# Kernel tuning notes

Hardware: AMD Instinct MI355X
Metric: run time of the kernel (lower is better)

## Reference

```python
import jax, jax.numpy as jnp
import numpy as np

B = 8
NUM_CLASSES = 80
STRIDES = (8, 16, 32, 64, 128)
HS = (96, 48, 24, 12, 6)
WS = (160, 80, 40, 20, 10)
IMG_H, IMG_W = 768, 1280
OCTAVE_SCALE = 4.0
LOC_THR = 0.01
SCORE_THR = 0.05
IOU_THR = 0.5
NMS_PRE = 1000
MAX_PER_IMG = 100
MAX_RATIO_ANCHOR = abs(float(np.log(1e-6)))        # anchor_coder wh_ratio_clip=1e-6
MAX_RATIO_BBOX = abs(float(np.log(16.0 / 1000.0)))  # bbox_coder default wh_ratio_clip
CLS_OFFSET = 4096.0  # > max image coord, separates classes for class-aware NMS


def setup_inputs():
    inp = {}
    k = 0
    for i, (h, w) in enumerate(zip(HS, WS)):
        for name, c in (("cls_score", NUM_CLASSES), ("bbox_pred", 4), ("shape_pred", 2), ("loc_pred", 1)):
            k += 1
            inp[f"{name}_{i}"] = jax.random.normal(jax.random.fold_in(jax.random.key(0), k), (B, c, h, w), dtype=jnp.float32)
    return inp


def _squares(h, w, stride):
    # mmdet square anchor generator: base size stride*octave_base_scale, ratio 1, center offset 0
    xs = jnp.arange(w, dtype=jnp.float32) * stride
    ys = jnp.arange(h, dtype=jnp.float32) * stride
    yy, xx = jnp.meshgrid(ys, xs, indexing="ij")
    half = 0.5 * OCTAVE_SCALE * stride
    return jnp.stack([xx - half, yy - half, xx + half, yy + half], -1).reshape(-1, 4)


def _delta2bbox(rois, deltas, max_ratio, max_shape=None):
    dx, dy = deltas[..., 0], deltas[..., 1]
    dw = jnp.clip(deltas[..., 2], -max_ratio, max_ratio)
    dh = jnp.clip(deltas[..., 3], -max_ratio, max_ratio)
    px = (rois[..., 0] + rois[..., 2]) * 0.5
    py = (rois[..., 1] + rois[..., 3]) * 0.5
    pw = rois[..., 2] - rois[..., 0]
    ph = rois[..., 3] - rois[..., 1]
    gx = px + pw * dx
    gy = py + ph * dy
    gw = pw * jnp.exp(dw)
    gh = ph * jnp.exp(dh)
    x1, y1 = gx - 0.5 * gw, gy - 0.5 * gh
    x2, y2 = gx + 0.5 * gw, gy + 0.5 * gh
    if max_shape is not None:
        x1 = jnp.clip(x1, 0.0, float(max_shape[1]))
        x2 = jnp.clip(x2, 0.0, float(max_shape[1]))
        y1 = jnp.clip(y1, 0.0, float(max_shape[0]))
        y2 = jnp.clip(y2, 0.0, float(max_shape[0]))
    return jnp.stack([x1, y1, x2, y2], -1)


def _level(cls, bbox, shp, loc, stride, h, w):
    b = cls.shape[0]
    # NOTE: double sigmoid is faithful to the original wrapper (it sigmoids twice)
    scores = jax.nn.sigmoid(jax.nn.sigmoid(jnp.transpose(cls, (0, 2, 3, 1)).reshape(b, -1, NUM_CLASSES)))
    mask = (jax.nn.sigmoid(loc) >= LOC_THR).astype(scores.dtype)
    mask = jnp.transpose(mask, (0, 2, 3, 1)).reshape(b, -1)  # num_anchors == 1
    scores = scores * mask[:, :, None]
    deltas = jnp.transpose(shp, (0, 2, 3, 1)).reshape(b, -1, 2)
    bdel = jnp.concatenate([jnp.zeros_like(deltas), deltas], axis=-1)  # [0,0,dw,dh]
    anchors = _delta2bbox(_squares(h, w, stride)[None], bdel, MAX_RATIO_ANCHOR)  # guided anchors
    bbox = jnp.transpose(bbox, (0, 2, 3, 1)).reshape(b, -1, 4)
    n = scores.shape[1]
    if n < NMS_PRE:  # pad_with_value
        pad = NMS_PRE - n
        scores = jnp.pad(scores, ((0, 0), (0, pad), (0, 0)))
        bbox = jnp.pad(bbox, ((0, 0), (0, pad), (0, 0)))
        anchors = jnp.pad(anchors, ((0, 0), (0, pad), (0, 0)))
    _, idx = jax.lax.top_k(scores.max(-1), NMS_PRE)
    scores = jnp.take_along_axis(scores, idx[:, :, None], axis=1)
    bbox = jnp.take_along_axis(bbox, idx[:, :, None], axis=1)
    anchors = jnp.take_along_axis(anchors, idx[:, :, None], axis=1)
    proposals = _delta2bbox(anchors, bbox, MAX_RATIO_BBOX, (IMG_H, IMG_W))
    return scores, proposals


def _iou_one_vs_all(box, boxes):
    lt = jnp.maximum(box[:2], boxes[:, :2])
    rb = jnp.minimum(box[2:], boxes[:, 2:])
    wh = jnp.clip(rb - lt, 0.0, None)
    inter = wh[:, 0] * wh[:, 1]
    a1 = (box[2] - box[0]) * (box[3] - box[1])
    a2 = (boxes[:, 2] - boxes[:, 0]) * (boxes[:, 3] - boxes[:, 1])
    return inter / (a1 + a2 - inter + 1e-6)


def _nms_single(scores, boxes):
    # class-aware greedy NMS (BatchedNMS semantics): scores [N,C], boxes [N,4]
    n, c = scores.shape
    s = jnp.where(scores > SCORE_THR, scores, 0.0).reshape(-1)  # [N*C]
    offs = (jnp.arange(c, dtype=boxes.dtype) * CLS_OFFSET)[None, :, None]
    cboxes = (boxes[:, None, :] + offs).reshape(-1, 4)  # class-offset boxes

    def step(sv, _):
        i = jnp.argmax(sv)
        sc = sv[i]
        keep = sc > 0.0
        iou = _iou_one_vs_all(cboxes[i], cboxes)
        sv = jnp.where(iou > IOU_THR, 0.0, sv)  # suppresses i itself too
        cls = jnp.where(keep, (i % c).astype(jnp.int32), -1)
        return sv, (boxes[i // c], sc, cls, keep)

    _, (ob, osc, ocls, okeep) = jax.lax.scan(step, s, None, length=MAX_PER_IMG)
    kf = okeep.astype(boxes.dtype)
    return okeep.sum().astype(jnp.int32), ob * kf[:, None], osc * kf, ocls


def _forward(tensors):
    mlvl_scores, mlvl_props = [], []
    for i in range(5):
        s, p = _level(tensors[4 * i], tensors[4 * i + 1], tensors[4 * i + 2], tensors[4 * i + 3],
                      STRIDES[i], HS[i], WS[i])
        mlvl_scores.append(s)
        mlvl_props.append(p)
    scores = jnp.concatenate(mlvl_scores, axis=1)   # [B, 5000, 80]
    props = jnp.concatenate(mlvl_props, axis=1)     # [B, 5000, 4]
    k = min(max(1000, NMS_PRE), scores.shape[1])
    _, idx = jax.lax.top_k(scores.max(-1), k)
    scores = jnp.take_along_axis(scores, idx[:, :, None], axis=1)
    props = jnp.take_along_axis(props, idx[:, :, None], axis=1)
    return jax.vmap(_nms_single)(scores, props)


def reference(cls_score_0, bbox_pred_0, shape_pred_0, loc_pred_0,
              cls_score_1, bbox_pred_1, shape_pred_1, loc_pred_1,
              cls_score_2, bbox_pred_2, shape_pred_2, loc_pred_2,
              cls_score_3, bbox_pred_3, shape_pred_3, loc_pred_3,
              cls_score_4, bbox_pred_4, shape_pred_4, loc_pred_4):
    tensors = [cls_score_0, bbox_pred_0, shape_pred_0, loc_pred_0,
               cls_score_1, bbox_pred_1, shape_pred_1, loc_pred_1,
               cls_score_2, bbox_pred_2, shape_pred_2, loc_pred_2,
               cls_score_3, bbox_pred_3, shape_pred_3, loc_pred_3,
               cls_score_4, bbox_pred_4, shape_pred_4, loc_pred_4]
    num_detected, proposals, out_scores, cls_id = _forward(tensors)
    return num_detected, proposals, out_scores, cls_id
```

## Files before the change

### kernel.cpp

```cpp
#include <hip/hip_runtime.h>
#include <stdint.h>

#define NCLS 80
#define BATCH 8
#define NA 20460
#define TOPK 1000
#define MAXPER 100
#define CAP 8
#define POOL 256
#define IMG_WF 1280.0f
#define IMG_HF 768.0f
#define CLS_OFF 4096.0f
#define MAX_RATIO_ANCHOR 13.815510557964274f
#define MAX_RATIO_BBOX   4.1351665567423557f

#define K2_HALF_UP (0.5 + 0x1p-25)

__constant__ int   c_lvoff[6]  = {0, 15360, 19200, 20160, 20400, 20460};
__constant__ int   c_lvoff4[6] = {0, 3840, 4800, 5040, 5100, 5115};
__constant__ int   c_lw[5]    = {160, 80, 40, 20, 10};
__constant__ int   c_lh[5]    = {96, 48, 24, 12, 6};
__constant__ float c_ls[5]    = {8.f, 16.f, 32.f, 64.f, 128.f};

struct InPtrs {
  const float* cls[5];
  const float* bbox[5];
  const float* shp[5];
  const float* loc[5];
};

__device__ __forceinline__ float sigf(float x) { return 1.0f / (1.0f + expf(-x)); }

__device__ __forceinline__ int wave_red_sum_i32(int v) {
  int t;
  t = __builtin_amdgcn_update_dpp(0, v, 0x111, 0xf, 0xf, false); v += t;
  t = __builtin_amdgcn_update_dpp(0, v, 0x112, 0xf, 0xf, false); v += t;
  t = __builtin_amdgcn_update_dpp(0, v, 0x114, 0xf, 0xf, false); v += t;
  t = __builtin_amdgcn_update_dpp(0, v, 0x118, 0xf, 0xf, false); v += t;
  t = __builtin_amdgcn_update_dpp(0, v, 0x142, 0xf, 0xf, false); v += t;
  t = __builtin_amdgcn_update_dpp(0, v, 0x143, 0xf, 0xf, false); v += t;
  return __builtin_amdgcn_readlane(v, 63);
}
__device__ __forceinline__ void wave_red_top2(unsigned m1, unsigned m2,
                                              unsigned& r1, unsigned& r2) {
#define T2STEP(ctrl) { \
    unsigned o1 = (unsigned)__builtin_amdgcn_update_dpp(0, (int)m1, ctrl, 0xf, 0xf, false); \
    unsigned o2 = (unsigned)__builtin_amdgcn_update_dpp(0, (int)m2, ctrl, 0xf, 0xf, false); \
    unsigned tm = min(m1, o1); \
    m1 = max(m1, o1); \
    m2 = max(tm, max(m2, o2)); }
  T2STEP(0x111) T2STEP(0x112) T2STEP(0x114) T2STEP(0x118) T2STEP(0x142) T2STEP(0x143)
#undef T2STEP
  r1 = (unsigned)__builtin_amdgcn_readlane((int)m1, 63);
  r2 = (unsigned)__builtin_amdgcn_readlane((int)m2, 63);
}

__global__ __launch_bounds__(256) void k_score(InPtrs P, unsigned* wkeys, unsigned* hist) {
  int gid = blockIdx.x * 256 + threadIdx.x;
  if (gid >= BATCH * (NA / 4)) return;
  int b = gid / (NA / 4);
  int q = gid - b * (NA / 4);
  int l = 0;
  while (q >= c_lvoff4[l + 1]) ++l;
  int hw = c_lh[l] * c_lw[l];
  int sp = (q - c_lvoff4[l]) * 4;
  const float4* cls = (const float4*)(P.cls[l] + (size_t)(b * NCLS) * hw + sp);
  int s4 = hw >> 2;
  float4 m = cls[0];
  for (int c = 1; c < NCLS; ++c) {
    float4 v = cls[(size_t)c * s4];
    m.x = fmaxf(m.x, v.x); m.y = fmaxf(m.y, v.y);
    m.z = fmaxf(m.z, v.z); m.w = fmaxf(m.w, v.w);
  }
  float4 lo = *(const float4*)(P.loc[l] + (size_t)b * hw + sp);
  float4 r;
  r.x = (sigf(lo.x) >= 0.01f) ? sigf(sigf(m.x)) : 0.0f;
  r.y = (sigf(lo.y) >= 0.01f) ? sigf(sigf(m.y)) : 0.0f;
  r.z = (sigf(lo.z) >= 0.01f) ? sigf(sigf(m.z)) : 0.0f;
  r.w = (sigf(lo.w) >= 0.01f) ? sigf(sigf(m.w)) : 0.0f;
  uint4 wq;
  wq.x = __float_as_uint(r.x) & 0x3FFFFFu;
  wq.y = __float_as_uint(r.y) & 0x3FFFFFu;
  wq.z = __float_as_uint(r.z) & 0x3FFFFFu;
  wq.w = __float_as_uint(r.w) & 0x3FFFFFu;
  ((uint4*)wkeys)[(size_t)b * (NA / 4) + q] = wq;
  unsigned* hb = hist + b * 2048;
  atomicAdd(&hb[wq.x >> 11], 1u);
  atomicAdd(&hb[wq.y >> 11], 1u);
  atomicAdd(&hb[wq.z >> 11], 1u);
  atomicAdd(&hb[wq.w >> 11], 1u);
}

__global__ __launch_bounds__(1024) void k_select(const unsigned* wkeys, const unsigned* hist,
                                                 int* sel) {
  int b = blockIdx.x;
  int tid = threadIdx.x;
  int wv = tid >> 6;
  int lane = tid & 63;
  __shared__ unsigned s_h[2048];
  __shared__ int s_wtot[16];
  __shared__ int s_res[2];
  __shared__ unsigned long long s_A[1024];
  __shared__ unsigned long long s_B[1024];

  const int NAq = NA / 4;
  unsigned w[20];
  #pragma unroll
  for (int k = 0; k < 5; ++k) {
    int q = tid * 5 + k;
    uint4 u = (q < NAq) ? ((const uint4*)wkeys)[(size_t)b * NAq + q]
                        : make_uint4(0u, 0u, 0u, 0u);
    w[k * 4 + 0] = u.x;
    w[k * 4 + 1] = u.y;
    w[k * 4 + 2] = u.z;
    w[k * 4 + 3] = u.w;
  }
  int lim = NA - tid * 20;
  lim = (lim < 0) ? 0 : ((lim > 20) ? 20 : lim);

  s_h[tid] = hist[b * 2048 + tid];
  s_h[tid + 1024] = hist[b * 2048 + 1024 + tid];
  __syncthreads();

  auto scanFind = [&](int target) {
    int b0 = 2047 - 2 * tid;
    int h0 = (int)s_h[b0];
    int h1 = (int)s_h[b0 - 1];
    int pair = h0 + h1;
    int incl = pair;
    #pragma unroll
    for (int o = 1; o < 64; o <<= 1) {
      int uu = __shfl_up(incl, o, 64);
      if (lane >= o) incl += uu;
    }
    if (lane == 63) s_wtot[wv] = incl;
    __syncthreads();
    int woff = 0;
    #pragma unroll
    for (int ww = 0; ww < 16; ++ww) woff += (ww < wv) ? s_wtot[ww] : 0;
    int excl = woff + incl - pair;
    if (excl < target && excl + h0 >= target) { s_res[0] = b0; s_res[1] = excl; }
    int e1 = excl + h0;
    if (e1 < target && e1 + h1 >= target) { s_res[0] = b0 - 1; s_res[1] = e1; }
    __syncthreads();
  };

  scanFind(TOPK);
  int B1 = s_res[0];
  int NGT1 = s_res[1];

  s_h[tid] = 0u; s_h[tid + 1024] = 0u;
  __syncthreads();
  #pragma unroll
  for (int k = 0; k < 20; ++k)
    if ((int)(w[k] >> 11) == B1) atomicAdd(&s_h[w[k] & 0x7FFu], 1u);
  __syncthreads();
  scanFind(TOPK - NGT1);
  unsigned V = ((unsigned)B1 << 11) | (unsigned)s_res[0];

  if (tid < 1024 - TOPK) s_A[TOPK + tid] = 0ull;

  int cgt = 0;
  #pragma unroll
  for (int k = 0; k < 20; ++k) cgt += (w[k] > V) ? 1 : 0;
  {
    int incl = cgt;
    #pragma unroll
    for (int o = 1; o < 64; o <<= 1) {
      int uu = __shfl_up(incl, o, 64);
      if (lane >= o) incl += uu;
    }
    if (lane == 63) s_wtot[wv] = incl;
    __syncthreads();
    int woff = 0, tot = 0;
    #pragma unroll
    for (int ww = 0; ww < 16; ++ww) { tot += s_wtot[ww]; woff += (ww < wv) ? s_wtot[ww] : 0; }
    int pos = woff + incl - cgt;
    #pragma unroll
    for (int k = 0; k < 20; ++k) {
      if (w[k] > V) {
        int i = tid * 20 + k;
        s_A[pos++] = ((unsigned long long)w[k] << 32) |
                     (unsigned long long)(0xFFFFFFFFu - (unsigned)i);
      }
    }
    int ngt = tot;
    int need = TOPK - ngt;
    __syncthreads();

    int ceq = 0;
    #pragma unroll
    for (int k = 0; k < 20; ++k) if (k < lim && w[k] == V) ++ceq;
    int incl2 = ceq;
    #pragma unroll
    for (int o = 1; o < 64; o <<= 1) {
      int uu = __shfl_up(incl2, o, 64);
      if (lane >= o) incl2 += uu;
    }
    if (lane == 63) s_wtot[wv] = incl2;
    __syncthreads();
    int woff2 = 0;
    #pragma unroll
    for (int ww = 0; ww < 16; ++ww) woff2 += (ww < wv) ? s_wtot[ww] : 0;
    int r = woff2 + incl2 - ceq;
    #pragma unroll
    for (int k = 0; k < 20; ++k) {
      if (k < lim && w[k] == V) {
        if (r < need) {
          int i = tid * 20 + k;
          s_A[ngt + r] = ((unsigned long long)V << 32) |
                         (unsigned long long)(0xFFFFFFFFu - (unsigned)i);
        }
        ++r;
      }
    }
  }
  __syncthreads();

  unsigned long long key = s_A[tid];
  int tog = 0;
  for (unsigned k = 2; k <= 1024; k <<= 1) {
    for (unsigned j = k >> 1; j > 0; j >>= 1) {
      unsigned long long other;
      if (j >= 64) {
        unsigned long long* cur = tog ? s_A : s_B;
        cur[tid] = key;
        __syncthreads();
        other = cur[tid ^ (int)j];
        tog ^= 1;
      } else {
        other = __shfl_xor(key, (int)j, 64);
      }
      bool takeMax = (((tid & (int)k) == 0) == ((tid & (int)j) == 0));
      unsigned long long mx = (key > other) ? key : other;
      unsigned long long mn = (key > other) ? other : key;
      key = takeMax ? mx : mn;
    }
  }
  if (tid < TOPK) {
    sel[b * TOPK + tid] = (int)(0xFFFFFFFFu - (unsigned)(key & 0xFFFFFFFFull));
  }
}

__global__ __launch_bounds__(256) void k_gather(InPtrs P, const int* sel, float* boxes, float* sv) {
  int wvi = threadIdx.x >> 6;
  int lane = threadIdx.x & 63;
  int wid = blockIdx.x * 4 + wvi;
  int b = wid / TOPK;
  int r = wid - b * TOPK;
  __shared__ float s_sc[4][NCLS];

  int a = sel[b * TOPK + r];
  int l = 0;
  while (a >= c_lvoff[l + 1]) ++l;
  int within = a - c_lvoff[l];
  int W = c_lw[l], H = c_lh[l];
  int y = within / W, x = within - y * W;
  int hw = H * W;
  int sp = within;
  float stride = c_ls[l];
  float px = (float)x * stride;
  float py = (float)y * stride;
  float pw = 4.0f * stride;

  const float* shp = P.shp[l];
  float dws = shp[(b * 2 + 0) * hw + sp];
  float dhs = shp[(b * 2 + 1) * hw + sp];
  dws = fminf(fmaxf(dws, -MAX_RATIO_ANCHOR), MAX_RATIO_ANCHOR);
  dhs = fminf(fmaxf(dhs, -MAX_RATIO_ANCHOR), MAX_RATIO_ANCHOR);
  float gw = pw * expf(dws);
  float gh = pw * expf(dhs);
  float ax1 = px - 0.5f * gw, ax2 = px + 0.5f * gw;
  float ay1 = py - 0.5f * gh, ay2 = py + 0.5f * gh;

  const float* bb = P.bbox[l];
  float dx = bb[(b * 4 + 0) * hw + sp];
  float dy = bb[(b * 4 + 1) * hw + sp];
  float dw = bb[(b * 4 + 2) * hw + sp];
  float dh = bb[(b * 4 + 3) * hw + sp];
  dw = fminf(fmaxf(dw, -MAX_RATIO_BBOX), MAX_RATIO_BBOX);
  dh = fminf(fmaxf(dh, -MAX_RATIO_BBOX), MAX_RATIO_BBOX);
  float px2 = (ax1 + ax2) * 0.5f, py2 = (ay1 + ay2) * 0.5f;
  float pw2 = ax2 - ax1, ph2 = ay2 - ay1;
  float gx = px2 + pw2 * dx, gy = py2 + ph2 * dy;
  float gw2 = pw2 * expf(dw), gh2 = ph2 * expf(dh);
  float x1 = fminf(fmaxf(gx - 0.5f * gw2, 0.0f), IMG_WF);
  float x2 = fminf(fmaxf(gx + 0.5f * gw2, 0.0f), IMG_WF);
  float y1 = fminf(fmaxf(gy - 0.5f * gh2, 0.0f), IMG_HF);
  float y2 = fminf(fmaxf(gy + 0.5f * gh2, 0.0f), IMG_HF);
  if (lane == 0) {
    float4 st; st.x = x1; st.y = y1; st.z = x2; st.w = y2;
    ((float4*)boxes)[b * TOPK + r] = st;
  }

  const float* cls = P.cls[l];
  float sl = sigf(P.loc[l][b * hw + sp]);
  bool mask = (sl >= 0.01f);
  int base = (b * NCLS) * hw + sp;
  for (int c = lane; c < NCLS; c += 64) {
    float vv = 0.0f;
    if (mask) {
      float s2 = sigf(sigf(cls[base + c * hw]));
      vv = (s2 > 0.05f) ? s2 : 0.0f;
    }
    s_sc[wvi][c] = vv;
  }
  __syncthreads();
  int t = threadIdx.x;
  if (t < NCLS) {
    int r0 = blockIdx.x * 4 - b * TOPK;
    float4 o; o.x = s_sc[0][t]; o.y = s_sc[1][t]; o.z = s_sc[2][t]; o.w = s_sc[3][t];
    *(float4*)(sv + ((size_t)(b * NCLS + t) * TOPK + r0)) = o;
  }
}

__global__ __launch_bounds__(256) void k_nms(const float* boxes, const float* sv,
                                             float* keptScore, int* keptRow, int* kc,
                                             const int* flags, const int* gbits, int cap) {
  int bc = blockIdx.x;
  if (flags && flags[bc] == 0) return;
  int b = bc / NCLS;
  int c = bc - b * NCLS;
  int tid = threadIdx.x;
  int wv = tid >> 6, lane = tid & 63;

  unsigned Glow = 0u;
  if (gbits) Glow = ((unsigned)gbits[b]) & 0x3FFFFFu;

  __shared__ float4 s_box[TOPK];
  __shared__ float  s_ard[TOPK];
  __shared__ unsigned long long s_p2[2][4];

  float x1[4], y1[4], x2[4], y2[4], ar[4];
  unsigned key[4];
  float off = (float)c * CLS_OFF;
  const float* svc = sv + (size_t)(b * NCLS + c) * TOPK;
  #pragma unroll
  for (int j = 0; j < 4; ++j) {
    int row = j * 256 + tid;
    if (row < TOPK) {
      float4 bo = ((const float4*)boxes)[b * TOPK + row];
      float a = bo.x + off, d = bo.y + off, e = bo.z + off, f = bo.w + off;
      x1[j] = a; y1[j] = d; x2[j] = e; y2[j] = f;
      ar[j] = (e - a) * (f - d);
      unsigned bits = __float_as_uint(svc[row]);
      key[j] = ((bits & 0x3FFFFFu) << 10) | (1023u - (unsigned)row);
      float sden = ar[j] + 1e-6f;
      bool deg = !((double)ar[j] > (double)sden * K2_HALF_UP);
      float4 sb; sb.x = a; sb.y = d; sb.z = e; sb.w = f;
      s_box[row] = sb;
      s_ard[row] = __uint_as_float(__float_as_uint(ar[j]) | (deg ? 0x80000000u : 0u));
    } else {
      x1[j] = y1[j] = x2[j] = y2[j] = ar[j] = 0.0f;
      key[j] = 0u;
    }
  }
  __syncthreads();

  int kept = 0;
  bool sticky = false;
  float* ks = keptScore + (size_t)(b * NCLS + c) * MAXPER;
  int*   kr = keptRow   + (size_t)(b * NCLS + c) * MAXPER;

  for (int round = 0; round < cap; ++round) {
    int par = round & 1;
    unsigned hi1 = max(key[0], key[1]), lo1 = min(key[0], key[1]);
    unsigned hi2 = max(key[2], key[3]), lo2 = min(key[2], key[3]);
    unsigned m1 = max(hi1, hi2);
    unsigned m2 = max(min(hi1, hi2), max(lo1, lo2));
    unsigned w1, w2;
    wave_red_top2(m1, m2, w1, w2);
    if (lane == 0) s_p2[par][wv] = ((unsigned long long)w1 << 32) | w2;
    __syncthreads();
    unsigned k0 = 0u, k1 = 0u;
    #pragma unroll
    for (int w = 0; w < 4; ++w) {
      unsigned long long pp = s_p2[par][w];
      unsigned p1 = (unsigned)(pp >> 32), p2 = (unsigned)pp;
      unsigned tm = min(k0, p1);
      k0 = max(k0, p1);
      k1 = max(tm, max(k1, p2));
    }
    if (k0 < 1024u) break;
    if ((k0 >> 10) < Glow) break;
    int brow1 = 1023 - (int)(k0 & 1023u);
    float bs1 = __uint_as_float(0x3F000000u | (k0 >> 10));
    float4 bb1 = s_box[brow1];
    unsigned au1 = __float_as_uint(s_ard[brow1]);
    bool deg1 = (au1 >> 31) != 0u;
    float ba1 = __uint_as_float(au1 & 0x7FFFFFFFu);
    if (tid == 0) { ks[kept] = bs1; kr[kept] = brow1; }
    kept++;
    if (deg1) { sticky = true; break; }
    if (kept >= cap) break;
    bool live2 = (k1 >= 1024u) && ((k1 >> 10) >= Glow);
    if (!live2) break;
    bool do2 = false, deg2 = false;
    float4 bb2; float ba2 = 0.0f;
    {
      int brow2 = 1023 - (int)(k1 & 1023u);
      float bs2 = __uint_as_float(0x3F000000u | (k1 >> 10));
      bb2 = s_box[brow2];
      unsigned au2 = __float_as_uint(s_ard[brow2]);
      deg2 = (au2 >> 31) != 0u;
      ba2 = __uint_as_float(au2 & 0x7FFFFFFFu);
      float ltx = fmaxf(bb1.x, bb2.x), rbx = fminf(bb1.z, bb2.z);
      float lty = fmaxf(bb1.y, bb2.y), rby = fminf(bb1.w, bb2.w);
      float w_ = fmaxf(rbx - ltx, 0.0f), h_ = fmaxf(rby - lty, 0.0f);
      float inter = w_ * h_;
      float denom = ((ba1 + ba2) - inter) + 1e-6f;
      if (!((double)inter > (double)denom * K2_HALF_UP)) {
        do2 = true;
        if (tid == 0) { ks[kept] = bs2; kr[kept] = brow2; }
        kept++;
      }
    }
    if (do2 && deg2) { sticky = true; break; }
    #pragma unroll
    for (int j = 0; j < 4; ++j) {
      {
        float ltx = fmaxf(bb1.x, x1[j]), rbx = fminf(bb1.z, x2[j]);
        float lty = fmaxf(bb1.y, y1[j]), rby = fminf(bb1.w, y2[j]);
        float w_ = fmaxf(rbx - ltx, 0.0f), h_ = fmaxf(rby - lty, 0.0f);
        float inter = w_ * h_;
        float denom = ((ba1 + ar[j]) - inter) + 1e-6f;
        if ((double)inter > (double)denom * K2_HALF_UP) key[j] = 0u;
      }
      if (do2) {
        float ltx = fmaxf(bb2.x, x1[j]), rbx = fminf(bb2.z, x2[j]);
        float lty = fmaxf(bb2.y, y1[j]), rby = fminf(bb2.w, y2[j]);
        float w_ = fmaxf(rbx - ltx, 0.0f), h_ = fmaxf(rby - lty, 0.0f);
        float inter = w_ * h_;
        float denom = ((ba2 + ar[j]) - inter) + 1e-6f;
        if ((double)inter > (double)denom * K2_HALF_UP) key[j] = 0u;
      }
    }
    if (kept >= cap) break;
  }
  if (tid == 0) kc[b * NCLS + c] = sticky ? -kept : kept;
}

__global__ __launch_bounds__(256) void k_cut(const float* keptScore, const int* kc,
                                             int* flags, int* gbits) {
  int b = blockIdx.x;
  int tid = threadIdx.x;
  int wv = tid >> 6, lane = tid & 63;
  __shared__ int s_abs[NCLS];
  __shared__ int s_neg[NCLS];
  __shared__ unsigned s_h[2048];
  __shared__ int s_wtot[4];
  __shared__ int s_res[2];
  __shared__ int s_tot[4];

  if (tid < NCLS) {
    int v = kc[b * NCLS + tid];
    s_abs[tid] = (v < 0) ? -v : v;
    s_neg[tid] = (v < 0) ? 1 : 0;
  }
  #pragma unroll
  for (int j = 0; j < 8; ++j) s_h[tid * 8 + j] = 0u;
  __syncthreads();

  unsigned vv[3] = {0u, 0u, 0u};
  #pragma unroll
  for (int t = 0; t < 3; ++t) {
    int e = tid + t * 256;
    if (e < NCLS * CAP) {
      int c = e / CAP, k = e - c * CAP;
      if (k < s_abs[c])
        vv[t] = __float_as_uint(keptScore[(size_t)b * NCLS * MAXPER + c * MAXPER + k])
                & 0x3FFFFFu;
    }
  }
  int live = ((vv[0] != 0u) ? 1 : 0) + ((vv[1] != 0u) ? 1 : 0) + ((vv[2] != 0u) ? 1 : 0);
  live = wave_red_sum_i32(live);
  if (lane == 0) s_tot[wv] = live;
  #pragma unroll
  for (int t = 0; t < 3; ++t) if (vv[t]) atomicAdd(&s_h[vv[t] >> 11], 1u);
  __syncthreads();
  int T = s_tot[0] + s_tot[1] + s_tot[2] + s_tot[3];

  auto scanFind = [&](int target) {
    int base = 2047 - 8 * tid;
    int h[8]; int loc = 0;
    #pragma unroll
    for (int j = 0; j < 8; ++j) { h[j] = (int)s_h[base - j]; loc += h[j]; }
    int incl = loc;
    #pragma unroll
    for (int o = 1; o < 64; o <<= 1) {
      int uu = __shfl_up(incl, o, 64);
      if (lane >= o) incl += uu;
    }
    if (lane == 63) s_wtot[wv] = incl;
    __syncthreads();
    int woff = 0;
    #pragma unroll
    for (int ww = 0; ww < 4; ++ww) woff += (ww < wv) ? s_wtot[ww] : 0;
    int e = woff + incl - loc;
    #pragma unroll
    for (int j = 0; j < 8; ++j) {
      if (e < target && e + h[j] >= target) { s_res[0] = base - j; s_res[1] = e; }
      e += h[j];
    }
    __syncthreads();
  };

  unsigned G = 0u;
  if (T >= MAXPER) {
    scanFind(MAXPER);
    int B1 = s_res[0], NGT1 = s_res[1];
    #pragma unroll
    for (int j = 0; j < 8; ++j) s_h[tid * 8 + j] = 0u;
    __syncthreads();
    #pragma unroll
    for (int t = 0; t < 3; ++t)
      if (vv[t] && (int)(vv[t] >> 11) == B1) atomicAdd(&s_h[vv[t] & 0x7FFu], 1u);
    __syncthreads();
    scanFind(MAXPER - NGT1);
    G = 0x3F000000u | ((unsigned)B1 << 11) | (unsigned)s_res[0];
  }
  if (tid == 0) gbits[b] = (int)G;
  if (tid < NCLS) {
    int f = 0;
    if (s_abs[tid] == CAP && !s_neg[tid]) {
      unsigned slast = __float_as_uint(
          keptScore[(size_t)b * NCLS * MAXPER + tid * MAXPER + (CAP - 1)]);
      if (slast >= G) f = 1;
    }
    flags[b * NCLS + tid] = f;
  }
}

__global__ __launch_bounds__(256) void k_merge(const float* boxes, const float* keptScore,
                                               const int* keptRow, const int* kc, float* out) {
  int b = blockIdx.x;
  int tid = threadIdx.x;
  int wv = tid >> 6, lane = tid & 63;
  __shared__ int s_kc[NCLS];
  __shared__ unsigned s_h[2048];
  __shared__ int s_wtot[4];
  __shared__ int s_res[2];
  __shared__ int s_tot[4];
  __shared__ int s_pos;
  __shared__ int s_sticky;
  __shared__ int s_navail;
  __shared__ unsigned long long s_pool[POOL];
  __shared__ unsigned long long s_sorted[POOL];

  for (int c = tid; c < NCLS; c += 256) s_kc[c] = kc[b * NCLS + c];
  if (tid == 0) { s_pos = 0; s_sticky = 0x7FFFFFFF; s_navail = 0; }
  for (int i = tid; i < POOL; i += 256) { s_pool[i] = 0ull; s_sorted[i] = 0ull; }
  #pragma unroll
  for (int j = 0; j < 8; ++j) s_h[tid * 8 + j] = 0u;
  __syncthreads();

  unsigned sc[32];
  #pragma unroll
  for (int s = 0; s < 32; ++s) {
    int i = tid + s * 256;
    unsigned vvv = 0u;
    if (i < NCLS * MAXPER) {
      int c = i / MAXPER, k = i - c * MAXPER;
      int kcv = s_kc[c];
      int ka = (kcv < 0) ? -kcv : kcv;
      if (k < ka)
        vvv = __float_as_uint(keptScore[(size_t)b * NCLS * MAXPER + i]) & 0x3FFFFFu;
    }
    sc[s] = vvv;
  }
  int live = 0;
  #pragma unroll
  for (int s = 0; s < 32; ++s) live += (sc[s] != 0u) ? 1 : 0;
  live = wave_red_sum_i32(live);
  if (lane == 0) s_tot[wv] = live;
  #pragma unroll
  for (int s = 0; s < 32; ++s) if (sc[s]) atomicAdd(&s_h[sc[s] >> 11], 1u);
  __syncthreads();
  int T = s_tot[0] + s_tot[1] + s_tot[2] + s_tot[3];

  auto scanFind = [&](int target) {
    int base = 2047 - 8 * tid;
    int h[8]; int loc = 0;
    #pragma unroll
    for (int j = 0; j < 8; ++j) { h[j] = (int)s_h[base - j]; loc += h[j]; }
    int incl = loc;
    #pragma unroll
    for (int o = 1; o < 64; o <<= 1) {
      int uu = __shfl_up(incl, o, 64);
      if (lane >= o) incl += uu;
    }
    if (lane == 63) s_wtot[wv] = incl;
    __syncthreads();
    int woff = 0;
    #pragma unroll
    for (int ww = 0; ww < 4; ++ww) woff += (ww < wv) ? s_wtot[ww] : 0;
    int e = woff + incl - loc;
    #pragma unroll
    for (int j = 0; j < 8; ++j) {
      if (e < target && e + h[j] >= target) { s_res[0] = base - j; s_res[1] = e; }
      e += h[j];
    }
    __syncthreads();
  };

  unsigned V = 1u;
  if (T > MAXPER) {
    scanFind(MAXPER);
    int B1 = s_res[0], NGT1 = s_res[1];
    #pragma unroll
    for (int j = 0; j < 8; ++j) s_h[tid * 8 + j] = 0u;
    __syncthreads();
    #pragma unroll
    for (int s = 0; s < 32; ++s)
      if (sc[s] && (int)(sc[s] >> 11) == B1) atomicAdd(&s_h[sc[s] & 0x7FFu], 1u);
    __syncthreads();
    scanFind(MAXPER - NGT1);
    V = ((unsigned)B1 << 11) | (unsigned)s_res[0];
  }

  #pragma unroll
  for (int s = 0; s < 32; ++s) {
    if (sc[s] >= V && sc[s] != 0u) {
      int i = tid + s * 256;
      int c = i / MAXPER, k = i - c * MAXPER;
      int kcv = s_kc[c];
      int ka = (kcv < 0) ? -kcv : kcv;
      unsigned st = (kcv < 0 && k == ka - 1) ? 1u : 0u;
      unsigned row = (unsigned)keptRow[(size_t)b * NCLS * MAXPER + i];
      unsigned flat = row * 80u + (unsigned)c;
      int p = atomicAdd(&s_pos, 1);
      if (p < POOL)
        s_pool[p] = ((unsigned long long)(0x3F000000u | sc[s]) << 32) |
                    (unsigned long long)(0x7FFFFFFFu - ((flat << 1) | st));
    }
  }
  __syncthreads();

  if (tid < POOL) {
    unsigned long long mykey = s_pool[tid];
    if (mykey != 0ull) {
      int rank = 0;
      #pragma unroll 8
      for (int s = 0; s < POOL; ++s) rank += (s_pool[s] > mykey) ? 1 : 0;
      s_sorted[rank] = mykey;
    }
  }
  __syncthreads();

  if (tid < MAXPER) {
    unsigned long long key = s_sorted[tid];
    if (key != 0ull) {
      atomicAdd(&s_navail, 1);
      if ((((unsigned)key) & 1u) == 0u) atomicMin(&s_sticky, tid);
    }
  }
  __syncthreads();
  int navail = s_navail;
  int p = s_sticky;
  int n = (p < navail) ? MAXPER : navail;

  if (tid == 0) out[b] = (float)n;
  const int OB = BATCH;
  const int OP = OB + BATCH * MAXPER * 4;
  const int OS = OP + BATCH * MAXPER;
  if (tid < MAXPER) {
    int k = tid;
    float bx0 = 0.f, bx1 = 0.f, bx2 = 0.f, bx3 = 0.f, scf = 0.f, cf = -1.0f;
    if (k < n) {
      int idx = (k > p) ? p : k;
      unsigned long long key = s_sorted[idx];
      unsigned flat = (0x7FFFFFFFu - (unsigned)key) >> 1;
      unsigned cls = flat % 80u;
      unsigned row = flat / 80u;
      float4 bo = ((const float4*)boxes)[b * TOPK + row];
      bx0 = bo.x; bx1 = bo.y; bx2 = bo.z; bx3 = bo.w;
      scf = __uint_as_float((unsigned)(key >> 32));
      cf = (float)cls;
    }
    float* po = out + OB + (size_t)(b * MAXPER + k) * 4;
    po[0] = bx0; po[1] = bx1; po[2] = bx2; po[3] = bx3;
    out[OP + b * MAXPER + k] = scf;
    out[OS + b * MAXPER + k] = cf;
  }
}

extern "C" void kernel_launch(void* const* d_in, const int* in_sizes, int n_in,
                              void* d_out, int out_size, void* d_ws, size_t ws_size,
                              hipStream_t stream) {
  InPtrs P;
  for (int l = 0; l < 5; ++l) {
    P.cls[l]  = (const float*)d_in[4 * l + 0];
    P.bbox[l] = (const float*)d_in[4 * l + 1];
    P.shp[l]  = (const float*)d_in[4 * l + 2];
    P.loc[l]  = (const float*)d_in[4 * l + 3];
  }
  unsigned* wkeys  = (unsigned*)d_ws;
  unsigned* hist   = wkeys + BATCH * NA;
  int*   sel       = (int*)(hist + BATCH * 2048);
  float* boxes     = (float*)(sel + BATCH * TOPK);
  float* sv        = boxes + BATCH * TOPK * 4;
  float* keptScore = sv + BATCH * NCLS * TOPK;
  int*   keptRow   = (int*)(keptScore + BATCH * NCLS * MAXPER);
  int*   kc        = keptRow + BATCH * NCLS * MAXPER;
  int*   flags     = kc + BATCH * NCLS;
  int*   gbits     = flags + BATCH * NCLS;
  float* out = (float*)d_out;

  hipMemsetAsync(hist, 0, BATCH * 2048 * sizeof(unsigned), stream);
  k_score<<<(BATCH * (NA / 4) + 255) / 256, 256, 0, stream>>>(P, wkeys, hist);
  k_select<<<BATCH, 1024, 0, stream>>>(wkeys, hist, sel);
  k_gather<<<BATCH * TOPK / 4, 256, 0, stream>>>(P, sel, boxes, sv);
  k_nms<<<BATCH * NCLS, 256, 0, stream>>>(boxes, sv, keptScore, keptRow, kc,
                                          (const int*)nullptr, (const int*)nullptr, CAP);
  k_cut<<<BATCH, 256, 0, stream>>>(keptScore, kc, flags, gbits);
  k_nms<<<BATCH * NCLS, 256, 0, stream>>>(boxes, sv, keptScore, keptRow, kc,
                                          flags, gbits, MAXPER);
  k_merge<<<BATCH, 256, 0, stream>>>(boxes, keptScore, keptRow, kc, out);
}
```

Before: 229.7 us.

## Replace radix-histogram threshold search with register binary search over key range

The global-atomic histogram in k_score, the hipMemsetAsync that cleared it, and the two-pass radix scan in k_select are removed. The top-1000 threshold is now found by binary search over the 22-bit key range, counting keys at or above each midpoint from registers with a wave reduction. k_merge's top-100 cutoff uses the same scheme. This drops the global atomics and one memset launch, but each block now runs about 22 block-wide reduction rounds, each ending in a __syncthreads.

```diff
diff --git a/kernel.cpp b/kernel.cpp
--- a/kernel.cpp
+++ b/kernel.cpp
@@ -16,6 +16,9 @@
 
 #define K2_HALF_UP (0.5 + 0x1p-25)
 
+#define WLIVE_LO 1u
+#define WLIVE_HI 0x3C0000u
+
 __constant__ int   c_lvoff[6]  = {0, 15360, 19200, 20160, 20400, 20460};
 __constant__ int   c_lvoff4[6] = {0, 3840, 4800, 5040, 5100, 5115};
 __constant__ int   c_lw[5]    = {160, 80, 40, 20, 10};
@@ -55,7 +58,7 @@
   r2 = (unsigned)__builtin_amdgcn_readlane((int)m2, 63);
 }
 
-__global__ __launch_bounds__(256) void k_score(InPtrs P, unsigned* wkeys, unsigned* hist) {
+__global__ __launch_bounds__(256) void k_score(InPtrs P, unsigned* wkeys) {
   int gid = blockIdx.x * 256 + threadIdx.x;
   if (gid >= BATCH * (NA / 4)) return;
   int b = gid / (NA / 4);
@@ -84,79 +87,54 @@
   wq.z = __float_as_uint(r.z) & 0x3FFFFFu;
   wq.w = __float_as_uint(r.w) & 0x3FFFFFu;
   ((uint4*)wkeys)[(size_t)b * (NA / 4) + q] = wq;
-  unsigned* hb = hist + b * 2048;
-  atomicAdd(&hb[wq.x >> 11], 1u);
-  atomicAdd(&hb[wq.y >> 11], 1u);
-  atomicAdd(&hb[wq.z >> 11], 1u);
-  atomicAdd(&hb[wq.w >> 11], 1u);
-}
-
-__global__ __launch_bounds__(1024) void k_select(const unsigned* wkeys, const unsigned* hist,
-                                                 int* sel) {
+}
+
+__global__ __launch_bounds__(1024) void k_select(const unsigned* wkeys, int* sel) {
   int b = blockIdx.x;
   int tid = threadIdx.x;
   int wv = tid >> 6;
   int lane = tid & 63;
-  __shared__ unsigned s_h[2048];
+  __shared__ int s_cnt[2][16];
   __shared__ int s_wtot[16];
-  __shared__ int s_res[2];
   __shared__ unsigned long long s_A[1024];
   __shared__ unsigned long long s_B[1024];
-
   const int NAq = NA / 4;
+
   unsigned w[20];
   #pragma unroll
   for (int k = 0; k < 5; ++k) {
     int q = tid * 5 + k;
     uint4 u = (q < NAq) ? ((const uint4*)wkeys)[(size_t)b * NAq + q]
                         : make_uint4(0u, 0u, 0u, 0u);
-    w[k * 4 + 0] = u.x;
-    w[k * 4 + 1] = u.y;
-    w[k * 4 + 2] = u.z;
-    w[k * 4 + 3] = u.w;
+    w[k * 4 + 0] = u.x; w[k * 4 + 1] = u.y; w[k * 4 + 2] = u.z; w[k * 4 + 3] = u.w;
   }
   int lim = NA - tid * 20;
   lim = (lim < 0) ? 0 : ((lim > 20) ? 20 : lim);
 
-  s_h[tid] = hist[b * 2048 + tid];
-  s_h[tid + 1024] = hist[b * 2048 + 1024 + tid];
-  __syncthreads();
-
-  auto scanFind = [&](int target) {
-    int b0 = 2047 - 2 * tid;
-    int h0 = (int)s_h[b0];
-    int h1 = (int)s_h[b0 - 1];
-    int pair = h0 + h1;
-    int incl = pair;
-    #pragma unroll
-    for (int o = 1; o < 64; o <<= 1) {
-      int uu = __shfl_up(incl, o, 64);
-      if (lane >= o) incl += uu;
-    }
-    if (lane == 63) s_wtot[wv] = incl;
-    __syncthreads();
-    int woff = 0;
-    #pragma unroll
-    for (int ww = 0; ww < 16; ++ww) woff += (ww < wv) ? s_wtot[ww] : 0;
-    int excl = woff + incl - pair;
-    if (excl < target && excl + h0 >= target) { s_res[0] = b0; s_res[1] = excl; }
-    int e1 = excl + h0;
-    if (e1 < target && e1 + h1 >= target) { s_res[0] = b0 - 1; s_res[1] = e1; }
-    __syncthreads();
+  int par = 0;
+  auto countGE = [&](unsigned mid) -> int {
+    int c = 0;
+    #pragma unroll
+    for (int k = 0; k < 20; ++k) c += (w[k] >= mid) ? 1 : 0;
+    c = wave_red_sum_i32(c);
+    if (lane == 0) s_cnt[par][wv] = c;
+    __syncthreads();
+    int tot = 0;
+    #pragma unroll
+    for (int i = 0; i < 16; ++i) tot += s_cnt[par][i];
+    par ^= 1;
+    return tot;
   };
 
-  scanFind(TOPK);
-  int B1 = s_res[0];
-  int NGT1 = s_res[1];
-
-  s_h[tid] = 0u; s_h[tid + 1024] = 0u;
-  __syncthreads();
-  #pragma unroll
-  for (int k = 0; k < 20; ++k)
-    if ((int)(w[k] >> 11) == B1) atomicAdd(&s_h[w[k] & 0x7FFu], 1u);
-  __syncthreads();
-  scanFind(TOPK - NGT1);
-  unsigned V = ((unsigned)B1 << 11) | (unsigned)s_res[0];
+  unsigned V = 0u;
+  if (countGE(WLIVE_LO) >= TOPK) {
+    unsigned lo = WLIVE_LO, hi = WLIVE_HI;
+    while (hi - lo > 1u) {
+      unsigned mid = lo + (hi - lo) / 2u;
+      if (countGE(mid) >= TOPK) lo = mid; else hi = mid;
+    }
+    V = lo;
+  }
 
   if (tid < 1024 - TOPK) s_A[TOPK + tid] = 0ull;
 
@@ -537,10 +515,7 @@
   int tid = threadIdx.x;
   int wv = tid >> 6, lane = tid & 63;
   __shared__ int s_kc[NCLS];
-  __shared__ unsigned s_h[2048];
-  __shared__ int s_wtot[4];
-  __shared__ int s_res[2];
-  __shared__ int s_tot[4];
+  __shared__ int s_cnt[2][4];
   __shared__ int s_pos;
   __shared__ int s_sticky;
   __shared__ int s_navail;
@@ -550,8 +525,6 @@
   for (int c = tid; c < NCLS; c += 256) s_kc[c] = kc[b * NCLS + c];
   if (tid == 0) { s_pos = 0; s_sticky = 0x7FFFFFFF; s_navail = 0; }
   for (int i = tid; i < POOL; i += 256) { s_pool[i] = 0ull; s_sorted[i] = 0ull; }
-  #pragma unroll
-  for (int j = 0; j < 8; ++j) s_h[tid * 8 + j] = 0u;
   __syncthreads();
 
   unsigned sc[32];
@@ -568,54 +541,29 @@
     }
     sc[s] = vvv;
   }
-  int live = 0;
-  #pragma unroll
-  for (int s = 0; s < 32; ++s) live += (sc[s] != 0u) ? 1 : 0;
-  live = wave_red_sum_i32(live);
-  if (lane == 0) s_tot[wv] = live;
-  #pragma unroll
-  for (int s = 0; s < 32; ++s) if (sc[s]) atomicAdd(&s_h[sc[s] >> 11], 1u);
-  __syncthreads();
-  int T = s_tot[0] + s_tot[1] + s_tot[2] + s_tot[3];
-
-  auto scanFind = [&](int target) {
-    int base = 2047 - 8 * tid;
-    int h[8]; int loc = 0;
-    #pragma unroll
-    for (int j = 0; j < 8; ++j) { h[j] = (int)s_h[base - j]; loc += h[j]; }
-    int incl = loc;
-    #pragma unroll
-    for (int o = 1; o < 64; o <<= 1) {
-      int uu = __shfl_up(incl, o, 64);
-      if (lane >= o) incl += uu;
-    }
-    if (lane == 63) s_wtot[wv] = incl;
-    __syncthreads();
-    int woff = 0;
-    #pragma unroll
-    for (int ww = 0; ww < 4; ++ww) woff += (ww < wv) ? s_wtot[ww] : 0;
-    int e = woff + incl - loc;
-    #pragma unroll
-    for (int j = 0; j < 8; ++j) {
-      if (e < target && e + h[j] >= target) { s_res[0] = base - j; s_res[1] = e; }
-      e += h[j];
-    }
-    __syncthreads();
+
+  int par = 0;
+  auto countGE = [&](unsigned mid) -> int {
+    int c = 0;
+    #pragma unroll
+    for (int s = 0; s < 32; ++s) c += (sc[s] >= mid) ? 1 : 0;
+    c = wave_red_sum_i32(c);
+    if (lane == 0) s_cnt[par][wv] = c;
+    __syncthreads();
+    int tot = s_cnt[par][0] + s_cnt[par][1] + s_cnt[par][2] + s_cnt[par][3];
+    par ^= 1;
+    return tot;
   };
 
-  unsigned V = 1u;
+  int T = countGE(WLIVE_LO);
+  unsigned V = WLIVE_LO;
   if (T > MAXPER) {
-    scanFind(MAXPER);
-    int B1 = s_res[0], NGT1 = s_res[1];
-    #pragma unroll
-    for (int j = 0; j < 8; ++j) s_h[tid * 8 + j] = 0u;
-    __syncthreads();
-    #pragma unroll
-    for (int s = 0; s < 32; ++s)
-      if (sc[s] && (int)(sc[s] >> 11) == B1) atomicAdd(&s_h[sc[s] & 0x7FFu], 1u);
-    __syncthreads();
-    scanFind(MAXPER - NGT1);
-    V = ((unsigned)B1 << 11) | (unsigned)s_res[0];
+    unsigned lo = WLIVE_LO, hi = WLIVE_HI;
+    while (hi - lo > 1u) {
+      unsigned mid = lo + (hi - lo) / 2u;
+      if (countGE(mid) >= MAXPER) lo = mid; else hi = mid;
+    }
+    V = lo;
   }
 
   #pragma unroll
@@ -695,8 +643,7 @@
     P.loc[l]  = (const float*)d_in[4 * l + 3];
   }
   unsigned* wkeys  = (unsigned*)d_ws;
-  unsigned* hist   = wkeys + BATCH * NA;
-  int*   sel       = (int*)(hist + BATCH * 2048);
+  int*   sel       = (int*)(wkeys + BATCH * NA);
   float* boxes     = (float*)(sel + BATCH * TOPK);
   float* sv        = boxes + BATCH * TOPK * 4;
   float* keptScore = sv + BATCH * NCLS * TOPK;
@@ -706,9 +653,8 @@
   int*   gbits     = flags + BATCH * NCLS;
   float* out = (float*)d_out;
 
-  hipMemsetAsync(hist, 0, BATCH * 2048 * sizeof(unsigned), stream);
-  k_score<<<(BATCH * (NA / 4) + 255) / 256, 256, 0, stream>>>(P, wkeys, hist);
-  k_select<<<BATCH, 1024, 0, stream>>>(wkeys, hist, sel);
+  k_score<<<(BATCH * (NA / 4) + 255) / 256, 256, 0, stream>>>(P, wkeys);
+  k_select<<<BATCH, 1024, 0, stream>>>(wkeys, sel);
   k_gather<<<BATCH * TOPK / 4, 256, 0, stream>>>(P, sel, boxes, sv);
   k_nms<<<BATCH * NCLS, 256, 0, stream>>>(boxes, sv, keptScore, keptRow, kc,
                                           (const int*)nullptr, (const int*)nullptr, CAP);
```

Result: faster. 214.0 us (-6.8%).
